# Kernel tuning notes

Hardware: AMD Instinct MI355X
Metric: run time of the kernel (lower is better)

The kernel has to match this reference:

```python
import jax, jax.numpy as jnp
import numpy as np

EPS = 1e-15
N, DIM, H, DH = 16384, 1024, 16, 64

# ---- stereographic (k<0, hyperbolic) math, per geoopt ----

def _sabs(k):
    return jnp.clip(jnp.abs(k), EPS, None)

def _tan_k(x, k):  # k < 0 branch of geoopt tan_k
    sk = jnp.sqrt(_sabs(k))
    return jnp.tanh(x * sk) / sk

def _artan_k(x, k):  # k < 0 branch of geoopt artan_k
    sk = jnp.sqrt(_sabs(k))
    return jnp.arctanh(jnp.clip(x * sk, -1.0 + 1e-7, 1.0 - 1e-7)) / sk

def _norm(x):
    return jnp.clip(jnp.sqrt(jnp.sum(x * x, -1, keepdims=True)), EPS, None)

def _project(x, k):
    n = _norm(x)
    maxnorm = (1.0 - 1e-5) / jnp.sqrt(_sabs(k))
    return jnp.where(n > maxnorm, x / n * maxnorm, x)

def _expmap0(u, k):
    un = _norm(u)
    return _tan_k(un, k) * u / un

def _logmap0(y, k):
    yn = _norm(y)
    return _artan_k(yn, k) * y / yn

def _mobius_add(x, y, k):
    x2 = jnp.sum(x * x, -1, keepdims=True)
    y2 = jnp.sum(y * y, -1, keepdims=True)
    xy = jnp.sum(x * y, -1, keepdims=True)
    num = (1 - 2 * k * xy - k * y2) * x + (1 + k * x2) * y
    den = jnp.clip(1 - 2 * k * xy + k * k * x2 * y2, EPS, None)
    return num / den

def _mobius_scalar_mul(r, x, k):
    xn = _norm(x)
    return _tan_k(r * _artan_k(xn, k), k) * x / xn

def _clamp_abs(x, eps):
    s = jnp.where(x >= 0, 1.0, -1.0)
    return s * jnp.clip(jnp.abs(x), eps, None)

# ---- StereographicLinear: mobius_matvec + mobius bias add, per head ----

def _stereo_linear(x, W, b, c, heads):
    n, fin = x.shape
    fout = W.shape[0]
    kk = c[None, :, None]  # per-head curvature
    u = _logmap0(x.reshape(n, heads, fin // heads), kk).reshape(n, fin)
    mu = (u @ W.T).reshape(n, heads, fout // heads)
    res = _project(_expmap0(mu, kk), kk)
    sb = _project(_expmap0(b.reshape(1, heads, fout // heads), kk), kk)
    res = _project(_mobius_add(res, sb, kk), kk)
    return res.reshape(n, fout)

# ---- GeometricLinearizedAttention ----

def _linear_attn(Q, K, V, mask, c):
    # Q, K, V: [H, n, d]; mask: [n]; c: [H]
    k = c[:, None, None]
    pt = jnp.clip(1.0 + k * jnp.sum(V * V, -1, keepdims=True), EPS, None)
    v1 = Q / pt                      # parallel_transport0back(V, Q)
    v2 = K / pt                      # parallel_transport0back(V, K)
    gamma = jnp.clip(2.0 / pt, EPS, None)  # lambda_x(V)
    den = _clamp_abs(gamma - 1.0, 1e-10)
    m = mask[None, :, None]
    x = gamma / den * V * m
    v1 = jax.nn.elu(v1) + 1.0
    v2 = den * (jax.nn.elu(v2) + 1.0) * m
    v2_sum = jnp.sum(v2, axis=-2)                    # [H, d]
    Dn = jnp.einsum('hnd,hd->hn', v1, v2_sum)
    D_inv = 1.0 / jnp.where(Dn == 0, 1e-5, Dn)
    ctx = jnp.einsum('hnd,hne->hde', v2, x)          # [H, d, d]
    Xo = jnp.einsum('hde,hnd,hn->hne', ctx, v1, D_inv)
    Xo = _project(Xo, k)
    Xo = _mobius_scalar_mul(0.5, Xo, k)
    return _project(Xo, k)


def setup_inputs() -> dict:
    key = jax.random.key(0)
    ks = jax.random.split(key, 11)
    hd = H * DH
    X = jax.random.normal(ks[0], (N, DIM), jnp.float32) * 0.05  # small norms -> inside Poincare ball
    mask = (jax.random.uniform(ks[1], (N,)) > 0.1).astype(jnp.float32)
    def lin(kk, fo, fi):
        return jax.random.normal(kk, (fo, fi), jnp.float32) / np.sqrt(fi).astype(np.float32)
    Wq = lin(ks[2], hd, DIM); bq = jnp.zeros((hd,), jnp.float32)
    Wk = lin(ks[3], hd, DIM); bk = jnp.zeros((hd,), jnp.float32)
    Wv = lin(ks[4], hd, DIM); bv = jax.random.normal(ks[5], (hd,), jnp.float32) * 0.01
    Wff = lin(ks[6], DIM, hd); bff = jax.random.normal(ks[7], (DIM,), jnp.float32) * 0.01
    c_v = -(jax.random.uniform(ks[8], (H,), jnp.float32) * 0.9 + 0.1)
    c_attn = -(jax.random.uniform(ks[9], (H,), jnp.float32) * 0.9 + 0.1)
    c_ff = -(jax.random.uniform(ks[10], (H,), jnp.float32) * 0.9 + 0.1)
    return dict(X=X, mask=mask, Wq=Wq, bq=bq, Wk=Wk, bk=bk, Wv=Wv, bv=bv,
                c_v=c_v, c_attn=c_attn, Wff=Wff, bff=bff, c_ff=c_ff)


def reference(X, mask, Wq, bq, Wk, bk, Wv, bv, c_v, c_attn, Wff, bff, c_ff):
    n = X.shape[0]
    def split(t):  # [n, H*DH] -> [H, n, DH]
        return t.reshape(n, H, DH).transpose(1, 0, 2)
    Q = split(X @ Wq.T + bq)
    K = split(X @ Wk.T + bk)
    V = split(_stereo_linear(X, Wv, bv, c_v, H))
    A = _linear_attn(Q, K, V, mask, c_attn)          # [H, n, DH]
    A = A.transpose(1, 0, 2).reshape(n, H * DH)
    return _stereo_linear(A, Wff, bff, c_ff, H)
```

## Files before the change

### kernel.cpp

```cpp
#include <hip/hip_runtime.h>
#include <math.h>
#include <stdint.h>

#define NTOK 16384
#define DIMF 1024
#define NH 16
#define DHD 64
#define NQK 2048

typedef _Float16 half_t;
typedef __attribute__((ext_vector_type(8))) _Float16 half8;
typedef __attribute__((ext_vector_type(4))) _Float16 half4;
typedef __attribute__((ext_vector_type(4))) float floatx4;

__device__ __forceinline__ float wsum(float v) {
  v += __shfl_xor(v, 32, 64);
  v += __shfl_xor(v, 16, 64);
  v += __shfl_xor(v, 8, 64);
  v += __shfl_xor(v, 4, 64);
  v += __shfl_xor(v, 2, 64);
  v += __shfl_xor(v, 1, 64);
  return v;
}

template <int CTRL>
__device__ __forceinline__ float dpp_add(float v) {
  int t = __builtin_amdgcn_update_dpp(0, __float_as_int(v), CTRL, 0xF, 0xF, true);
  return v + __int_as_float(t);
}
__device__ __forceinline__ float wsum16(float v) {
  v = dpp_add<0xB1>(v);
  v = dpp_add<0x4E>(v);
  v = dpp_add<0x124>(v);
  v = dpp_add<0x128>(v);
  return v;
}

__device__ __forceinline__ float frcp(float x) { return __builtin_amdgcn_rcpf(x); }
__device__ __forceinline__ float fexp(float x) { return __expf(x); }
__device__ __forceinline__ float flog(float x) { return __logf(x); }
__device__ __forceinline__ float ftanh_pos(float x) {
  float e = fexp(2.f * x);
  return 1.f - 2.f * frcp(e + 1.f);
}
__device__ __forceinline__ float fatanh01(float t) {
  return 0.5f * flog((1.f + t) * frcp(1.f - t));
}

__device__ __forceinline__ void gload16(const void* g, void* lds) {
  __builtin_amdgcn_global_load_lds(
      (const __attribute__((address_space(1))) uint32_t*)(uintptr_t)g,
      (__attribute__((address_space(3))) uint32_t*)(uintptr_t)lds, 16, 0, 0);
}

struct EpiArgs {
  const float* sb;
  const float* y2;
  const float* c_st;
  const float* c_at;
  const float* mask;
  half_t* Qh;
  half_t* Kh;
  half_t* v2T;
  half_t* xT;
  float* v2sum;
  int qstride;
};

template <int MODE, typename OutT>
__global__ __launch_bounds__(512, 2) void gemm_f16(const half_t* __restrict__ A,
                                                   const half_t* __restrict__ B,
                                                   const float* __restrict__ bias,
                                                   OutT* __restrict__ C,
                                                   int M, int Nn, int K, EpiArgs ep) {
  __shared__ half_t sA[2][256 * 64];
  __shared__ half_t sB[2][256 * 64];
  const int tid = threadIdx.x;
  const int lane = tid & 63;
  const int w = tid >> 6;
  const int wm = w >> 2;
  const int wn = w & 3;

  int gx = gridDim.x;
  int nwg = gx * gridDim.y;
  int lin = blockIdx.y * gx + blockIdx.x;
  int bx = blockIdx.x, by = blockIdx.y;
  if ((nwg & 7) == 0) {
    int cpx = nwg >> 3;
    int swz = (lin & 7) * cpx + (lin >> 3);
    bx = swz % gx;
    by = swz / gx;
  }
  const int n0 = bx * 256;
  const int m0 = by * 256;

  const half_t* pA[2];
  const half_t* pB[2];
#pragma unroll
  for (int t = 0; t < 2; ++t) {
    int g = 2 * w + t;
    pA[t] = A + (size_t)(m0 + g * 16 + (lane & 15)) * K + ((lane >> 4) << 3);
    pB[t] = B + (size_t)(n0 + g * 16 + (lane & 15)) * K + ((lane >> 4) << 3);
  }

  auto stageA = [&](int KS, int T, half_t* buf) {
#pragma unroll
    for (int t = 0; t < 2; ++t)
      gload16(pA[t] + KS * 32 + T * 64, buf + (KS * 16 + 2 * w + t) * 512);
  };
  auto stageB = [&](int KS, int T, half_t* buf) {
#pragma unroll
    for (int t = 0; t < 2; ++t)
      gload16(pB[t] + KS * 32 + T * 64, buf + (KS * 16 + 2 * w + t) * 512);
  };

  floatx4 acc[8][4];
#pragma unroll
  for (int i = 0; i < 8; ++i)
#pragma unroll
    for (int j = 0; j < 4; ++j) acc[i][j] = (floatx4){0.f, 0.f, 0.f, 0.f};

  const int NTt = K >> 6;

  stageA(0, 0, &sA[0][0]);
  stageB(0, 0, &sB[0][0]);
  stageA(1, 0, &sA[0][0]);
  stageB(1, 0, &sB[0][0]);
  stageA(0, 1, &sA[1][0]);
  stageB(0, 1, &sB[1][0]);
  stageA(1, 1, &sA[1][0]);
  asm volatile("s_waitcnt vmcnt(6)" ::: "memory");
  __builtin_amdgcn_s_barrier();

  for (int kt = 0; kt < NTt; ++kt) {
    const int c = kt & 1;
    half_t* sAc = c ? &sA[1][0] : &sA[0][0];
    half_t* sBc = c ? &sB[1][0] : &sB[0][0];
    half_t* sBn = c ? &sB[0][0] : &sB[1][0];
    half8 af[8], b0, b1;

#pragma unroll
    for (int i = 0; i < 8; ++i)
      af[i] = *(const half8*)&sAc[(wm * 8 + i) * 512 + lane * 8];
    b0 = *(const half8*)&sBc[(wn * 4 + 0) * 512 + lane * 8];
    b1 = *(const half8*)&sBc[(wn * 4 + 1) * 512 + lane * 8];
    if (kt + 1 < NTt) stageB(1, kt + 1, sBn);
    __builtin_amdgcn_s_barrier();
    __builtin_amdgcn_s_setprio(1);
#pragma unroll
    for (int i = 0; i < 8; ++i) {
      acc[i][0] = __builtin_amdgcn_mfma_f32_16x16x32_f16(af[i], b0, acc[i][0], 0, 0, 0);
      acc[i][1] = __builtin_amdgcn_mfma_f32_16x16x32_f16(af[i], b1, acc[i][1], 0, 0, 0);
    }
    __builtin_amdgcn_s_setprio(0);
    __builtin_amdgcn_s_barrier();

    b0 = *(const half8*)&sBc[(wn * 4 + 2) * 512 + lane * 8];
    b1 = *(const half8*)&sBc[(wn * 4 + 3) * 512 + lane * 8];
    if (kt + 2 < NTt) stageA(0, kt + 2, sAc);
    __builtin_amdgcn_s_barrier();
    __builtin_amdgcn_s_setprio(1);
#pragma unroll
    for (int i = 0; i < 8; ++i) {
      acc[i][2] = __builtin_amdgcn_mfma_f32_16x16x32_f16(af[i], b0, acc[i][2], 0, 0, 0);
      acc[i][3] = __builtin_amdgcn_mfma_f32_16x16x32_f16(af[i], b1, acc[i][3], 0, 0, 0);
    }
    __builtin_amdgcn_s_setprio(0);
    __builtin_amdgcn_s_barrier();

#pragma unroll
    for (int i = 0; i < 8; ++i)
      af[i] = *(const half8*)&sAc[(16 + wm * 8 + i) * 512 + lane * 8];
    b0 = *(const half8*)&sBc[(16 + wn * 4 + 0) * 512 + lane * 8];
    b1 = *(const half8*)&sBc[(16 + wn * 4 + 1) * 512 + lane * 8];
    if (kt + 2 < NTt) stageB(0, kt + 2, sBc);
    __builtin_amdgcn_s_barrier();
    __builtin_amdgcn_s_setprio(1);
#pragma unroll
    for (int i = 0; i < 8; ++i) {
      acc[i][0] = __builtin_amdgcn_mfma_f32_16x16x32_f16(af[i], b0, acc[i][0], 0, 0, 0);
      acc[i][1] = __builtin_amdgcn_mfma_f32_16x16x32_f16(af[i], b1, acc[i][1], 0, 0, 0);
    }
    __builtin_amdgcn_s_setprio(0);
    __builtin_amdgcn_s_barrier();

    b0 = *(const half8*)&sBc[(16 + wn * 4 + 2) * 512 + lane * 8];
    b1 = *(const half8*)&sBc[(16 + wn * 4 + 3) * 512 + lane * 8];
    if (kt + 2 < NTt) stageA(1, kt + 2, sAc);
    __builtin_amdgcn_s_barrier();
    __builtin_amdgcn_s_setprio(1);
#pragma unroll
    for (int i = 0; i < 8; ++i) {
      acc[i][2] = __builtin_amdgcn_mfma_f32_16x16x32_f16(af[i], b0, acc[i][2], 0, 0, 0);
      acc[i][3] = __builtin_amdgcn_mfma_f32_16x16x32_f16(af[i], b1, acc[i][3], 0, 0, 0);
    }
    __builtin_amdgcn_s_setprio(0);
    if (kt < NTt - 2)
      asm volatile("s_waitcnt vmcnt(6)" ::: "memory");
    else
      asm volatile("s_waitcnt vmcnt(0)" ::: "memory");
    __builtin_amdgcn_s_barrier();
  }

  const int e = lane & 15;
  const int quad = lane >> 4;

  if constexpr (MODE == 0) {
#pragma unroll
    for (int j = 0; j < 4; ++j) {
      int col = n0 + wn * 64 + j * 16 + e;
      float bv = bias ? bias[col] : 0.f;
#pragma unroll
      for (int i = 0; i < 8; ++i) {
        int row = m0 + wm * 128 + i * 16 + quad * 4;
#pragma unroll
        for (int r = 0; r < 4; ++r)
          C[(size_t)(row + r) * Nn + col] = (OutT)(acc[i][j][r] + bv);
      }
    }
  } else {
    const int hb = n0 + wn * 64;
    const int h = hb >> 6;
    const float kst = ep.c_st[h];
    const float sk = sqrtf(fmaxf(fabsf(kst), 1e-15f));
    const float rsk = frcp(sk);
    const float maxn = (1.f - 1e-5f) * rsk;
    const float mx2 = maxn * maxn;
    float sbj[4];
#pragma unroll
    for (int j = 0; j < 4; ++j) sbj[j] = ep.sb[hb + j * 16 + e];
    const float y2h = ep.y2[h];
    float ka = 0.f, v2acc[4] = {0.f, 0.f, 0.f, 0.f};
    if constexpr (MODE == 1) ka = ep.c_at[h];
    const int rowbase = m0 + wm * 128;

#pragma unroll
    for (int i = 0; i < 8; ++i) {
      half4 v2s[4], xs[4];
#pragma unroll
      for (int r = 0; r < 4; ++r) {
        const int row = rowbase + i * 16 + quad * 4 + r;
        float qraw[4], kraw[4];
        float mrow = 0.f;
        size_t qb = 0;
        if constexpr (MODE == 1) {
          qb = (size_t)row * ep.qstride + hb + e;
#pragma unroll
          for (int j = 0; j < 4; ++j) {
            qraw[j] = (float)ep.Qh[qb + j * 16];
            kraw[j] = (float)ep.Kh[qb + j * 16];
          }
          mrow = ep.mask[row];
        }
        float s = 0.f, dp = 0.f;
#pragma unroll
        for (int j = 0; j < 4; ++j) {
          float mv = acc[i][j][r];
          s += mv * mv;
          dp += mv * sbj[j];
        }
        s = wsum16(s);
        dp = wsum16(dp);
        float un = fmaxf(sqrtf(s), 1e-15f);
        float tn = ftanh_pos(un * sk) * rsk;
        float f = tn * frcp(un);
        float rn = fmaxf(tn, 1e-15f);
        if (rn > maxn) { f *= maxn * frcp(rn); rn = maxn; }
        float xy = dp * f;
        float x2 = rn * rn;
        float num1 = 1.f - 2.f * kst * xy - kst * y2h;
        float num2 = 1.f + kst * x2;
        float den = fmaxf(1.f - 2.f * kst * xy + kst * kst * x2 * y2h, 1e-15f);
        float rden = frcp(den);
        float c1 = num1 * f * rden;
        float c2 = num2 * rden;
        float o[4];
        float os = 0.f;
#pragma unroll
        for (int j = 0; j < 4; ++j) {
          o[j] = c1 * acc[i][j][r] + c2 * sbj[j];
          os += o[j] * o[j];
        }
        os = wsum16(os);
        float on = fmaxf(sqrtf(os), 1e-15f);
        if (on > maxn) {
          float sc = maxn * frcp(on);
#pragma unroll
          for (int j = 0; j < 4; ++j) o[j] *= sc;
        }
        if constexpr (MODE == 2) {
#pragma unroll
          for (int j = 0; j < 4; ++j)
            C[(size_t)row * Nn + hb + j * 16 + e] = (OutT)o[j];
        } else {
          float vn2 = fminf(os, mx2);
          float pt = fmaxf(1.f + ka * vn2, 1e-15f);
          float rpt = frcp(pt);
          float gamma = fmaxf(2.f * rpt, 1e-15f);
          float gm1 = gamma - 1.f;
          float aden = fmaxf(fabsf(gm1), 1e-10f);
          float den2 = (gm1 >= 0.f) ? aden : -aden;
          float xsc = gamma * frcp(den2) * mrow;
#pragma unroll
          for (int j = 0; j < 4; ++j) {
            float q = qraw[j] * rpt;
            float v1 = (q > 0.f) ? (q + 1.f) : fexp(q);
            ep.Qh[qb + j * 16] = (half_t)v1;
            float kv = kraw[j] * rpt;
            float v2 = den2 * ((kv > 0.f) ? (kv + 1.f) : fexp(kv)) * mrow;
            v2acc[j] += v2;
            v2s[j][r] = (half_t)v2;
            xs[j][r] = (half_t)(xsc * o[j]);
          }
        }
      }
      if constexpr (MODE == 1) {
        const size_t tb0 = (size_t)(rowbase + i * 16 + quad * 4);
#pragma unroll
        for (int j = 0; j < 4; ++j) {
          size_t tb = (size_t)(hb + j * 16 + e) * NTOK + tb0;
          *(half4*)&ep.v2T[tb] = v2s[j];
          *(half4*)&ep.xT[tb] = xs[j];
        }
      }
    }
    if constexpr (MODE == 1) {
#pragma unroll
      for (int j = 0; j < 4; ++j) {
        float t = v2acc[j];
        t += __shfl_xor(t, 16, 64);
        t += __shfl_xor(t, 32, 64);
        if (quad == 0) atomicAdd(&ep.v2sum[h * DHD + j * 16 + e], t);
      }
    }
  }
}

struct WPack {
  const float* w[4];
  half_t* h[4];
};
__global__ __launch_bounds__(256) void convert_w_kernel(WPack pk) {
  int wi = blockIdx.y;
  const float* w = pk.w[wi];
  half_t* ph = pk.h[wi];
  int i = (blockIdx.x * 256 + threadIdx.x) * 4;
  float4 v = *(const float4*)&w[i];
  half4 hh = {(half_t)v.x, (half_t)v.y, (half_t)v.z, (half_t)v.w};
  *(half4*)&ph[i] = hh;
}

__global__ __launch_bounds__(128) void prep_sb_kernel(const float* __restrict__ bv,
                                                      const float* __restrict__ cv,
                                                      const float* __restrict__ bf,
                                                      const float* __restrict__ cf,
                                                      const float* __restrict__ bq,
                                                      const float* __restrict__ bk,
                                                      float* __restrict__ sbV,
                                                      float* __restrict__ y2V,
                                                      float* __restrict__ sbF,
                                                      float* __restrict__ y2F,
                                                      float* __restrict__ bqk) {
  int tid = threadIdx.x;
  for (int i = tid; i < 1024; i += 128) {
    bqk[i] = bq[i];
    bqk[1024 + i] = bk[i];
  }
  int wv = tid >> 6;
  int lane = tid & 63;
  const float* b = wv ? bf : bv;
  const float* c = wv ? cf : cv;
  float* sb = wv ? sbF : sbV;
  float* y2 = wv ? y2F : y2V;
  for (int h = 0; h < NH; ++h) {
    float k = c[h];
    float sk = sqrtf(fmaxf(fabsf(k), 1e-15f));
    float rsk = frcp(sk);
    float maxn = (1.f - 1e-5f) * rsk;
    float bb = b[h * DHD + lane];
    float bs = wsum(bb * bb);
    float bn = fmaxf(sqrtf(bs), 1e-15f);
    float tb = ftanh_pos(bn * sk) * rsk;
    float sv = tb * frcp(bn) * bb;
    float sbn = fmaxf(tb, 1e-15f);
    if (sbn > maxn) { sv *= maxn * frcp(sbn); sbn = maxn; }
    sb[h * DHD + lane] = sv;
    if (lane == 0) y2[h] = sbn * sbn;
  }
}

__global__ __launch_bounds__(256) void prep_kernel(const float* __restrict__ X,
                                                   half_t* __restrict__ Xh,
                                                   half_t* __restrict__ U,
                                                   const float* __restrict__ c) {
  int lane = threadIdx.x & 63;
  int wid = blockIdx.x * 4 + (threadIdx.x >> 6);
  int nw = gridDim.x * 4;
  int sub = lane >> 4;
  for (int row = wid; row < NTOK; row += nw) {
#pragma unroll
    for (int ch = 0; ch < 4; ++ch) {
      int h = ch * 4 + sub;
      int idx = row * DIMF + ch * 256 + lane * 4;
      float4 x = *(const float4*)&X[idx];
      float s = x.x * x.x + x.y * x.y + x.z * x.z + x.w * x.w;
      s = wsum16(s);
      float k = c[h];
      float sk = sqrtf(fmaxf(fabsf(k), 1e-15f));
      float yn = fmaxf(sqrtf(s), 1e-15f);
      float t = fminf(yn * sk, 1.f - 1e-7f);
      float f = fatanh01(t) * frcp(sk) * frcp(yn);
      half4 xh4 = {(half_t)x.x, (half_t)x.y, (half_t)x.z, (half_t)x.w};
      *(half4*)&Xh[idx] = xh4;
      half4 u4 = {(half_t)(x.x * f), (half_t)(x.y * f), (half_t)(x.z * f), (half_t)(x.w * f)};
      *(half4*)&U[idx] = u4;
    }
  }
}

__global__ __launch_bounds__(256) void attn_pass2(const half_t* __restrict__ v2T,
                                                  const half_t* __restrict__ xT,
                                                  float* __restrict__ ctxT) {
  __shared__ float red[4096];
  int tid = threadIdx.x;
  int h = blockIdx.y;
  for (int i = tid; i < 4096; i += 256) red[i] = 0.f;
  __syncthreads();
  int lane = tid & 63;
  int w = tid >> 6;
  int m = lane & 15;
  int q = lane >> 4;
  const half_t* xb = xT + (size_t)h * 64 * NTOK;
  const half_t* vb = v2T + (size_t)h * 64 * NTOK;
  floatx4 acc[4][4];
#pragma unroll
  for (int i = 0; i < 4; ++i)
#pragma unroll
    for (int j = 0; j < 4; ++j) acc[i][j] = (floatx4){0.f, 0.f, 0.f, 0.f};

  int tok0 = blockIdx.x * 512 + w * 32 + q * 8;
#pragma unroll
  for (int c = 0; c < 4; ++c) {
    int tk = tok0 + c * 128;
    half8 af[4], bf[4];
#pragma unroll
    for (int i = 0; i < 4; ++i)
      af[i] = *(const half8*)&xb[(size_t)(i * 16 + m) * NTOK + tk];
#pragma unroll
    for (int j = 0; j < 4; ++j)
      bf[j] = *(const half8*)&vb[(size_t)(j * 16 + m) * NTOK + tk];
#pragma unroll
    for (int i = 0; i < 4; ++i)
#pragma unroll
      for (int j = 0; j < 4; ++j)
        acc[i][j] = __builtin_amdgcn_mfma_f32_16x16x32_f16(af[i], bf[j], acc[i][j], 0, 0, 0);
  }
#pragma unroll
  for (int i = 0; i < 4; ++i)
#pragma unroll
    for (int j = 0; j < 4; ++j)
#pragma unroll
      for (int r = 0; r < 4; ++r) {
        int e = i * 16 + q * 4 + r;
        int d = j * 16 + m;
        atomicAdd(&red[e * 64 + d], acc[i][j][r]);
      }
  __syncthreads();
  float* dst = ctxT + (size_t)h * 4096;
  for (int i = tid; i < 4096; i += 256) atomicAdd(&dst[i], red[i]);
}

__global__ __launch_bounds__(256) void attn_pass3m(const half_t* __restrict__ v1h,
                                                   const float* __restrict__ ctxT,
                                                   const float* __restrict__ v2sum,
                                                   const float* __restrict__ c_at,
                                                   const float* __restrict__ c_ff,
                                                   half_t* __restrict__ Uff,
                                                   int sv1) {
  __shared__ half_t sctx[8 * 64 * 8];
  int tid = threadIdx.x;
  int h = blockIdx.y;
  int m0 = blockIdx.x * 64;
  for (int ci = tid; ci < 512; ci += 256) {
    int t = ci >> 6, l = ci & 63;
    int j = t & 3, ks = t >> 2;
    int e2 = j * 16 + (l & 15);
    int d = ks * 32 + (l >> 4) * 8;
    const float* src = &ctxT[h * 4096 + e2 * 64 + d];
    half8 hh;
#pragma unroll
    for (int q = 0; q < 8; ++q) hh[q] = (half_t)src[q];
    *(half8*)&sctx[ci * 8] = hh;
  }
  __syncthreads();

  int lane = tid & 63;
  int w = tid >> 6;
  int quad = lane >> 4;
  int e = lane & 15;

  const half_t* ap = v1h + (size_t)(m0 + w * 16 + e) * sv1 + h * DHD + quad * 8;
  half8 a0 = *(const half8*)ap;
  half8 a1 = *(const half8*)(ap + 32);

  const float* vsp = v2sum + h * DHD + quad * 8;
  float4 va = *(const float4*)&vsp[0];
  float4 vb = *(const float4*)&vsp[4];
  float4 vc = *(const float4*)&vsp[32];
  float4 vd = *(const float4*)&vsp[36];
  float dn = (float)a0[0] * va.x + (float)a0[1] * va.y + (float)a0[2] * va.z + (float)a0[3] * va.w +
             (float)a0[4] * vb.x + (float)a0[5] * vb.y + (float)a0[6] * vb.z + (float)a0[7] * vb.w +
             (float)a1[0] * vc.x + (float)a1[1] * vc.y + (float)a1[2] * vc.z + (float)a1[3] * vc.w +
             (float)a1[4] * vd.x + (float)a1[5] * vd.y + (float)a1[6] * vd.z + (float)a1[7] * vd.w;
  dn += __shfl_xor(dn, 16, 64);
  dn += __shfl_xor(dn, 32, 64);
  float di = frcp((dn == 0.f) ? 1e-5f : dn);

  floatx4 acc[4];
#pragma unroll
  for (int j = 0; j < 4; ++j) acc[j] = (floatx4){0.f, 0.f, 0.f, 0.f};
#pragma unroll
  for (int j = 0; j < 4; ++j) {
    half8 b0 = *(const half8*)&sctx[((0 * 4 + j) * 64 + lane) * 8];
    half8 b1 = *(const half8*)&sctx[((1 * 4 + j) * 64 + lane) * 8];
    acc[j] = __builtin_amdgcn_mfma_f32_16x16x32_f16(a0, b0, acc[j], 0, 0, 0);
    acc[j] = __builtin_amdgcn_mfma_f32_16x16x32_f16(a1, b1, acc[j], 0, 0, 0);
  }

  float ka = c_at[h];
  float sk_a = sqrtf(fmaxf(fabsf(ka), 1e-15f));
  float rsk_a = frcp(sk_a);
  float maxn_a = (1.f - 1e-5f) * rsk_a;
  float kf = c_ff[h];
  float sk_f = sqrtf(fmaxf(fabsf(kf), 1e-15f));
  float rsk_f = frcp(sk_f);

#pragma unroll
  for (int r = 0; r < 4; ++r) {
    float Di = __shfl(di, quad * 4 + r, 64);
    float v0 = acc[0][r], v1 = acc[1][r], v2 = acc[2][r], v3 = acc[3][r];
    float s = v0 * v0 + v1 * v1 + v2 * v2 + v3 * v3;
    s = wsum16(s);
    int row = m0 + w * 16 + quad * 4 + r;
    float f = Di;
    float xn = fmaxf(sqrtf(s) * Di, 1e-15f);
    if (xn > maxn_a) { f *= maxn_a * frcp(xn); xn = maxn_a; }
    float t = fminf(xn * sk_a, 1.f - 1e-7f);
    float ar = fatanh01(t) * rsk_a;
    float tk = ftanh_pos(0.5f * ar * sk_a) * rsk_a;
    f *= tk * frcp(xn);
    float nn = tk;
    if (nn > maxn_a) { f *= maxn_a * frcp(nn); nn = maxn_a; }
    float fn = fmaxf(nn, 1e-15f);
    float t2 = fminf(fn * sk_f, 1.f - 1e-7f);
    float ar2 = fatanh01(t2) * rsk_f;
    f *= ar2 * frcp(fn);
    size_t base = (size_t)row * DIMF + h * DHD + e;
    Uff[base + 0] = (half_t)(v0 * f);
    Uff[base + 16] = (half_t)(v1 * f);
    Uff[base + 32] = (half_t)(v2 * f);
    Uff[base + 48] = (half_t)(v3 * f);
  }
}

extern "C" void kernel_launch(void* const* d_in, const int* in_sizes, int n_in,
                              void* d_out, int out_size, void* d_ws, size_t ws_size,
                              hipStream_t stream) {
  const float* X = (const float*)d_in[0];
  const float* mask = (const float*)d_in[1];
  const float* Wq = (const float*)d_in[2];
  const float* bq = (const float*)d_in[3];
  const float* Wk = (const float*)d_in[4];
  const float* bk = (const float*)d_in[5];
  const float* Wv = (const float*)d_in[6];
  const float* bv = (const float*)d_in[7];
  const float* c_v = (const float*)d_in[8];
  const float* c_at = (const float*)d_in[9];
  const float* Wff = (const float*)d_in[10];
  const float* bff = (const float*)d_in[11];
  const float* c_ff = (const float*)d_in[12];
  float* out = (float*)d_out;

  const size_t NE = (size_t)NTOK * DIMF;
  float* v2sum = (float*)d_ws;
  float* ctxT = v2sum + 1024;
  float* sbV = ctxT + 65536;
  float* sbF = sbV + 1024;
  float* y2V = sbF + 1024;
  float* y2F = y2V + 16;
  float* bqk = y2F + 16;
  half_t* H1 = (half_t*)(bqk + 2048);
  half_t* H2 = H1 + NE;
  half_t* HQK = H2 + NE;
  half_t* V2T = HQK + 2 * NE;
  half_t* XT = V2T + NE;
  half_t* Wh0 = XT + NE;

  WPack pk;
  pk.w[0] = Wq; pk.w[1] = Wk; pk.w[2] = Wv; pk.w[3] = Wff;
  for (int i = 0; i < 4; ++i) pk.h[i] = Wh0 + (size_t)i * DIMF * DIMF;

  EpiArgs epN{};
  EpiArgs epV{sbV, y2V, c_v, c_at, mask, HQK, HQK + 1024, V2T, XT, v2sum, NQK};
  EpiArgs epF{sbF, y2F, c_ff, nullptr, nullptr, nullptr, nullptr, nullptr, nullptr, nullptr, 0};

  convert_w_kernel<<<dim3(1024, 4), 256, 0, stream>>>(pk);
  prep_sb_kernel<<<1, 128, 0, stream>>>(bv, c_v, bff, c_ff, bq, bk, sbV, y2V, sbF, y2F, bqk);
  prep_kernel<<<512, 256, 0, stream>>>(X, H1, H2, c_v);
  hipMemsetAsync(v2sum, 0, (1024 + 65536) * sizeof(float), stream);
  gemm_f16<0, half_t><<<dim3(NQK / 256, NTOK / 256), 512, 0, stream>>>(
      H1, pk.h[0], bqk, HQK, NTOK, NQK, DIMF, epN);
  gemm_f16<1, half_t><<<dim3(DIMF / 256, NTOK / 256), 512, 0, stream>>>(
      H2, pk.h[2], nullptr, (half_t*)nullptr, NTOK, DIMF, DIMF, epV);
  attn_pass2<<<dim3(NTOK / 512, NH), 256, 0, stream>>>(V2T, XT, ctxT);
  attn_pass3m<<<dim3(NTOK / 64, NH), 256, 0, stream>>>(HQK, ctxT, v2sum, c_at, c_ff, H1, NQK);
  gemm_f16<2, float><<<dim3(DIMF / 256, NTOK / 256), 512, 0, stream>>>(
      H1, pk.h[3], nullptr, out, NTOK, DIMF, DIMF, epF);
}
```

Baseline: 500.3 us.

## Reorder GEMM inner loop into 4x4 MFMA subtiles and de-atomicize attention reduction

```diff
diff --git a/kernel.cpp b/kernel.cpp
--- a/kernel.cpp
+++ b/kernel.cpp
@@ -126,9 +126,9 @@
   stageB(0, 0, &sB[0][0]);
   stageA(1, 0, &sA[0][0]);
   stageB(1, 0, &sB[0][0]);
+  stageB(0, 1, &sB[1][0]);
   stageA(0, 1, &sA[1][0]);
-  stageB(0, 1, &sB[1][0]);
-  stageA(1, 1, &sA[1][0]);
+  stageB(1, 1, &sB[1][0]);
   asm volatile("s_waitcnt vmcnt(6)" ::: "memory");
   __builtin_amdgcn_s_barrier();
 
@@ -136,64 +136,68 @@
     const int c = kt & 1;
     half_t* sAc = c ? &sA[1][0] : &sA[0][0];
     half_t* sBc = c ? &sB[1][0] : &sB[0][0];
-    half_t* sBn = c ? &sB[0][0] : &sB[1][0];
-    half8 af[8], b0, b1;
-
-#pragma unroll
-    for (int i = 0; i < 8; ++i)
-      af[i] = *(const half8*)&sAc[(wm * 8 + i) * 512 + lane * 8];
-    b0 = *(const half8*)&sBc[(wn * 4 + 0) * 512 + lane * 8];
-    b1 = *(const half8*)&sBc[(wn * 4 + 1) * 512 + lane * 8];
-    if (kt + 1 < NTt) stageB(1, kt + 1, sBn);
+    half_t* sAn = c ? &sA[0][0] : &sA[1][0];
+    half8 a[4], bb[4];
+
+#pragma unroll
+    for (int i = 0; i < 4; ++i)
+      a[i] = *(const half8*)&sAc[(wm * 8 + i) * 512 + lane * 8];
+#pragma unroll
+    for (int j = 0; j < 4; ++j)
+      bb[j] = *(const half8*)&sBc[(wn * 4 + j) * 512 + lane * 8];
+    if (kt + 1 < NTt) stageA(1, kt + 1, sAn);
     __builtin_amdgcn_s_barrier();
     __builtin_amdgcn_s_setprio(1);
 #pragma unroll
-    for (int i = 0; i < 8; ++i) {
-      acc[i][0] = __builtin_amdgcn_mfma_f32_16x16x32_f16(af[i], b0, acc[i][0], 0, 0, 0);
-      acc[i][1] = __builtin_amdgcn_mfma_f32_16x16x32_f16(af[i], b1, acc[i][1], 0, 0, 0);
-    }
+    for (int i = 0; i < 4; ++i)
+#pragma unroll
+      for (int j = 0; j < 4; ++j)
+        acc[i][j] = __builtin_amdgcn_mfma_f32_16x16x32_f16(a[i], bb[j], acc[i][j], 0, 0, 0);
     __builtin_amdgcn_s_setprio(0);
     __builtin_amdgcn_s_barrier();
 
-    b0 = *(const half8*)&sBc[(wn * 4 + 2) * 512 + lane * 8];
-    b1 = *(const half8*)&sBc[(wn * 4 + 3) * 512 + lane * 8];
+#pragma unroll
+    for (int i = 0; i < 4; ++i)
+      a[i] = *(const half8*)&sAc[(wm * 8 + 4 + i) * 512 + lane * 8];
+    if (kt + 2 < NTt) stageB(0, kt + 2, sBc);
+    __builtin_amdgcn_s_barrier();
+    __builtin_amdgcn_s_setprio(1);
+#pragma unroll
+    for (int i = 0; i < 4; ++i)
+#pragma unroll
+      for (int j = 0; j < 4; ++j)
+        acc[4 + i][j] = __builtin_amdgcn_mfma_f32_16x16x32_f16(a[i], bb[j], acc[4 + i][j], 0, 0, 0);
+    __builtin_amdgcn_s_setprio(0);
+    __builtin_amdgcn_s_barrier();
+
+#pragma unroll
+    for (int i = 0; i < 4; ++i)
+      a[i] = *(const half8*)&sAc[(16 + wm * 8 + i) * 512 + lane * 8];
+#pragma unroll
+    for (int j = 0; j < 4; ++j)
+      bb[j] = *(const half8*)&sBc[(16 + wn * 4 + j) * 512 + lane * 8];
     if (kt + 2 < NTt) stageA(0, kt + 2, sAc);
     __builtin_amdgcn_s_barrier();
     __builtin_amdgcn_s_setprio(1);
 #pragma unroll
-    for (int i = 0; i < 8; ++i) {
-      acc[i][2] = __builtin_amdgcn_mfma_f32_16x16x32_f16(af[i], b0, acc[i][2], 0, 0, 0);
-      acc[i][3] = __builtin_amdgcn_mfma_f32_16x16x32_f16(af[i], b1, acc[i][3], 0, 0, 0);
-    }
+    for (int i = 0; i < 4; ++i)
+#pragma unroll
+      for (int j = 0; j < 4; ++j)
+        acc[i][j] = __builtin_amdgcn_mfma_f32_16x16x32_f16(a[i], bb[j], acc[i][j], 0, 0, 0);
     __builtin_amdgcn_s_setprio(0);
     __builtin_amdgcn_s_barrier();
 
 #pragma unroll
-    for (int i = 0; i < 8; ++i)
-      af[i] = *(const half8*)&sAc[(16 + wm * 8 + i) * 512 + lane * 8];
-    b0 = *(const half8*)&sBc[(16 + wn * 4 + 0) * 512 + lane * 8];
-    b1 = *(const half8*)&sBc[(16 + wn * 4 + 1) * 512 + lane * 8];
-    if (kt + 2 < NTt) stageB(0, kt + 2, sBc);
+    for (int i = 0; i < 4; ++i)
+      a[i] = *(const half8*)&sAc[(16 + wm * 8 + 4 + i) * 512 + lane * 8];
+    if (kt + 2 < NTt) stageB(1, kt + 2, sBc);
     __builtin_amdgcn_s_barrier();
     __builtin_amdgcn_s_setprio(1);
 #pragma unroll
-    for (int i = 0; i < 8; ++i) {
-      acc[i][0] = __builtin_amdgcn_mfma_f32_16x16x32_f16(af[i], b0, acc[i][0], 0, 0, 0);
-      acc[i][1] = __builtin_amdgcn_mfma_f32_16x16x32_f16(af[i], b1, acc[i][1], 0, 0, 0);
-    }
-    __builtin_amdgcn_s_setprio(0);
-    __builtin_amdgcn_s_barrier();
-
-    b0 = *(const half8*)&sBc[(16 + wn * 4 + 2) * 512 + lane * 8];
-    b1 = *(const half8*)&sBc[(16 + wn * 4 + 3) * 512 + lane * 8];
-    if (kt + 2 < NTt) stageA(1, kt + 2, sAc);
-    __builtin_amdgcn_s_barrier();
-    __builtin_amdgcn_s_setprio(1);
-#pragma unroll
-    for (int i = 0; i < 8; ++i) {
-      acc[i][2] = __builtin_amdgcn_mfma_f32_16x16x32_f16(af[i], b0, acc[i][2], 0, 0, 0);
-      acc[i][3] = __builtin_amdgcn_mfma_f32_16x16x32_f16(af[i], b1, acc[i][3], 0, 0, 0);
-    }
+    for (int i = 0; i < 4; ++i)
+#pragma unroll
+      for (int j = 0; j < 4; ++j)
+        acc[4 + i][j] = __builtin_amdgcn_mfma_f32_16x16x32_f16(a[i], bb[j], acc[4 + i][j], 0, 0, 0);
     __builtin_amdgcn_s_setprio(0);
     if (kt < NTt - 2)
       asm volatile("s_waitcnt vmcnt(6)" ::: "memory");
@@ -421,11 +425,9 @@
 __global__ __launch_bounds__(256) void attn_pass2(const half_t* __restrict__ v2T,
                                                   const half_t* __restrict__ xT,
                                                   float* __restrict__ ctxT) {
-  __shared__ float red[4096];
+  __shared__ float red[4][4096];
   int tid = threadIdx.x;
   int h = blockIdx.y;
-  for (int i = tid; i < 4096; i += 256) red[i] = 0.f;
-  __syncthreads();
   int lane = tid & 63;
   int w = tid >> 6;
   int m = lane & 15;
@@ -438,9 +440,9 @@
 #pragma unroll
     for (int j = 0; j < 4; ++j) acc[i][j] = (floatx4){0.f, 0.f, 0.f, 0.f};
 
-  int tok0 = blockIdx.x * 512 + w * 32 + q * 8;
-#pragma unroll
-  for (int c = 0; c < 4; ++c) {
+  int tok0 = blockIdx.x * 1024 + w * 32 + q * 8;
+#pragma unroll
+  for (int c = 0; c < 8; ++c) {
     int tk = tok0 + c * 128;
     half8 af[4], bf[4];
 #pragma unroll
@@ -460,14 +462,14 @@
 #pragma unroll
     for (int j = 0; j < 4; ++j)
 #pragma unroll
-      for (int r = 0; r < 4; ++r) {
-        int e = i * 16 + q * 4 + r;
-        int d = j * 16 + m;
-        atomicAdd(&red[e * 64 + d], acc[i][j][r]);
-      }
+      for (int r = 0; r < 4; ++r)
+        red[w][(i * 16 + q * 4 + r) * 64 + j * 16 + m] = acc[i][j][r];
   __syncthreads();
   float* dst = ctxT + (size_t)h * 4096;
-  for (int i = tid; i < 4096; i += 256) atomicAdd(&dst[i], red[i]);
+  for (int idx = tid; idx < 4096; idx += 256) {
+    float s = (red[0][idx] + red[1][idx]) + (red[2][idx] + red[3][idx]);
+    atomicAdd(&dst[idx], s);
+  }
 }
 
 __global__ __launch_bounds__(256) void attn_pass3m(const half_t* __restrict__ v1h,
@@ -612,7 +614,7 @@
       H1, pk.h[0], bqk, HQK, NTOK, NQK, DIMF, epN);
   gemm_f16<1, half_t><<<dim3(DIMF / 256, NTOK / 256), 512, 0, stream>>>(
       H2, pk.h[2], nullptr, (half_t*)nullptr, NTOK, DIMF, DIMF, epV);
-  attn_pass2<<<dim3(NTOK / 512, NH), 256, 0, stream>>>(V2T, XT, ctxT);
+  attn_pass2<<<dim3(NTOK / 1024, NH), 256, 0, stream>>>(V2T, XT, ctxT);
   attn_pass3m<<<dim3(NTOK / 64, NH), 256, 0, stream>>>(HQK, ctxT, v2sum, c_at, c_ff, H1, NQK);
   gemm_f16<2, float><<<dim3(DIMF / 256, NTOK / 256), 512, 0, stream>>>(
       H1, pk.h[3], nullptr, out, NTOK, DIMF, DIMF, epF);
```

Result: slower. 605.2 us (+21.0%).
